# Optimization experiments

Hardware: AMD Instinct MI355X
Metric: run time of the kernel (lower is better)

## Reference

```python
import jax, jax.numpy as jnp
import numpy as np

NUM_TYPES = 4
IN_DIM = 128
HID_DIM = 256
OUT_DIM = 128
NUM_NODES = 100000


def setup_inputs() -> dict:
    key = jax.random.key(0)
    k_x, k_t, k_w1, k_b1, k_w2, k_b2 = jax.random.split(key, 6)
    raw_features = jax.random.normal(k_x, (NUM_NODES, IN_DIM), dtype=jnp.float32)
    node_type = jax.random.randint(k_t, (NUM_NODES,), 0, NUM_TYPES, dtype=jnp.int64)
    # stacked per-type MLP params (Kaiming-ish scale like torch Linear defaults)
    W1 = jax.random.uniform(k_w1, (NUM_TYPES, IN_DIM, HID_DIM), dtype=jnp.float32,
                            minval=-1.0, maxval=1.0) / np.sqrt(IN_DIM)
    b1 = jax.random.uniform(k_b1, (NUM_TYPES, HID_DIM), dtype=jnp.float32,
                            minval=-1.0, maxval=1.0) / np.sqrt(IN_DIM)
    W2 = jax.random.uniform(k_w2, (NUM_TYPES, HID_DIM, OUT_DIM), dtype=jnp.float32,
                            minval=-1.0, maxval=1.0) / np.sqrt(HID_DIM)
    b2 = jax.random.uniform(k_b2, (NUM_TYPES, OUT_DIM), dtype=jnp.float32,
                            minval=-1.0, maxval=1.0) / np.sqrt(HID_DIM)
    return {"raw_features": raw_features, "node_type": node_type,
            "W1": W1, "b1": b1, "W2": W2, "b2": b2}


def reference(raw_features, node_type, W1, b1, W2, b2):
    # Run every expert on every node (num_types is tiny), then select per node.
    # h: [types, nodes, hidden]
    h = jax.nn.relu(jnp.einsum('ni,tih->tnh', raw_features, W1) + b1[:, None, :])
    # out_all: [types, nodes, out]
    out_all = jnp.einsum('tnh,tho->tno', h, W2) + b2[:, None, :]
    # select expert output matching each node's type -> [nodes, out]
    encoded = out_all[node_type, jnp.arange(raw_features.shape[0])]
    return encoded
```

## Files before the change

### kernel.cpp

```cpp
#include <hip/hip_runtime.h>
#include <hip/hip_bf16.h>

typedef float f32x4 __attribute__((ext_vector_type(4)));
typedef short short8 __attribute__((ext_vector_type(8)));

#define NTYPES 4


static __device__ __forceinline__ unsigned short f2bf(float f) {
  union { float f; unsigned int u; } v; v.f = f;
  unsigned int u = v.u;
  unsigned int r = u + 0x7FFFu + ((u >> 16) & 1u);
  return (unsigned short)(r >> 16);
}

static __device__ __forceinline__ unsigned int pkbf(float a, float b) {
  __hip_bfloat162 h = __float22bfloat162_rn(make_float2(a, b));
  union { __hip_bfloat162 h; unsigned int u; } v; v.h = h;
  return v.u;
}

__global__ __launch_bounds__(256) void k_prep(const float* __restrict__ W1,
                                              const float* __restrict__ W2,
                                              unsigned short* __restrict__ W1T,
                                              unsigned short* __restrict__ W2T,
                                              int* __restrict__ meta) {
  __shared__ unsigned short s[64][72];
  const int tid = threadIdx.x;
  const int b = blockIdx.x;
  if (b == 0 && tid < 16) meta[tid] = 0;
  const int bb = b & 31;
  const int t = bb >> 3, ti = bb & 7;
  const float* src; unsigned short* dst; int scols, tr, tc;
  if (b < 32) { src = W1 + t * 32768; dst = W1T + t * 32768; scols = 256; tr = ti >> 2; tc = ti & 3; }
  else        { src = W2 + t * 32768; dst = W2T + t * 32768; scols = 128; tr = ti >> 1; tc = ti & 1; }
  const int srows = 32768 / scols;
  const int r0 = tid >> 4, c4 = (tid & 15) << 2;
  #pragma unroll
  for (int i = 0; i < 4; ++i) {
    int r = tr * 64 + i * 16 + r0;
    float4 v = *(const float4*)(src + r * scols + tc * 64 + c4);
    s[i * 16 + r0][c4 + 0] = f2bf(v.x);
    s[i * 16 + r0][c4 + 1] = f2bf(v.y);
    s[i * 16 + r0][c4 + 2] = f2bf(v.z);
    s[i * 16 + r0][c4 + 3] = f2bf(v.w);
  }
  __syncthreads();
  #pragma unroll
  for (int i = 0; i < 4; ++i) {
    int orow = i * 16 + r0;
    ushort4 u;
    u.x = s[c4 + 0][orow];
    u.y = s[c4 + 1][orow];
    u.z = s[c4 + 2][orow];
    u.w = s[c4 + 3][orow];
    *(ushort4*)(dst + (tc * 64 + orow) * srows + tr * 64 + c4) = u;
  }
}

__global__ __launch_bounds__(256) void k_hist(const int* __restrict__ NT, int n,
                                              int* __restrict__ meta) {
  __shared__ int c[NTYPES];
  if (threadIdx.x < NTYPES) c[threadIdx.x] = 0;
  __syncthreads();
  int i = blockIdx.x * 256 + threadIdx.x;
  if (i < n) atomicAdd(&c[NT[i]], 1);
  __syncthreads();
  if (threadIdx.x < NTYPES && c[threadIdx.x] > 0)
    atomicAdd(&meta[threadIdx.x], c[threadIdx.x]);
}

__global__ __launch_bounds__(256) void k_scatter(const int* __restrict__ NT, int n,
                                                 int* __restrict__ meta,
                                                 int* __restrict__ perm) {
  __shared__ int cnt[NTYPES];
  __shared__ int cbase[NTYPES];
  __shared__ int sb[NTYPES + 1];
  if (threadIdx.x < NTYPES) cnt[threadIdx.x] = 0;
  if (threadIdx.x == 0) {
    int b = 0; sb[0] = 0;
    for (int t = 0; t < NTYPES; ++t) {
      b += (meta[t] + 63) & ~63;
      sb[t + 1] = b;
    }
  }
  __syncthreads();
  int i = blockIdx.x * 256 + threadIdx.x;
  int t = 0, r = 0;
  bool valid = (i < n);
  if (valid) { t = NT[i]; r = atomicAdd(&cnt[t], 1); }
  __syncthreads();
  if (threadIdx.x < NTYPES)
    cbase[threadIdx.x] = atomicAdd(&meta[4 + threadIdx.x], cnt[threadIdx.x]);
  __syncthreads();
  if (valid) perm[sb[t] + cbase[t] + r] = i;
  if (blockIdx.x == 0) {
    if (threadIdx.x <= NTYPES) meta[8 + threadIdx.x] = sb[threadIdx.x];
    int tt = threadIdx.x >> 6, j = threadIdx.x & 63;
    int p = sb[tt] + meta[tt] + j;
    if (p < sb[tt + 1]) perm[p] = -1;
  }
}

__global__ __launch_bounds__(256, 1) void k_mlpw(
    const float* __restrict__ X, const int* __restrict__ perm,
    const int* __restrict__ meta,
    const unsigned short* __restrict__ W1T, const unsigned short* __restrict__ W2T,
    const float* __restrict__ B1, const float* __restrict__ B2,
    float* __restrict__ OUT, float* __restrict__ dump) {
  __shared__ __align__(16) unsigned char x_lds[16384];
  __shared__ __align__(16) unsigned char h_lds[32768];

  const int tid = threadIdx.x;
  const int l  = tid & 63, w = tid >> 6;
  const int lo = l & 15,  hi = l >> 4;

  const int t  = blockIdx.x >> 7;
  const int lb = blockIdx.x & 127;
  const int g0 = meta[8 + t] >> 6;
  const int g1 = meta[9 + t] >> 6;
  const int nt = g1 - g0 - lb;
  if (nt <= 0) return;
  const int cnt = (nt + 127) >> 7;

  const int gr = tid >> 2;
  const int gq = tid & 3;

  int pm = perm[(g0 + lb) * 64 + gr];
  float4 xv[8];
  #pragma unroll
  for (int i = 0; i < 8; ++i) xv[i] = make_float4(0.f, 0.f, 0.f, 0.f);
  if (pm >= 0) {
    const float4* s = (const float4*)(X + (size_t)pm * 128 + gq * 32);
    #pragma unroll
    for (int i = 0; i < 8; ++i) xv[i] = s[i];
  }

  const unsigned short* w1t = W1T + (t << 15);
  const unsigned short* w2t = W2T + (t << 15);
  short8 a1[4][4];
  #pragma unroll
  for (int ks = 0; ks < 4; ++ks)
    #pragma unroll
    for (int m = 0; m < 4; ++m)
      a1[ks][m] = *(const short8*)(w1t + (w * 64 + m * 16 + lo) * 128 + ks * 32 + hi * 8);
  short8 a2[8][2];
  #pragma unroll
  for (int ks = 0; ks < 8; ++ks)
    #pragma unroll
    for (int mo = 0; mo < 2; ++mo)
      a2[ks][mo] = *(const short8*)(w2t + (w * 32 + mo * 16 + lo) * 256 + ks * 32 + hi * 8);
  f32x4 bb1[4], bb2[2];
  #pragma unroll
  for (int m = 0; m < 4; ++m)
    bb1[m] = *(const f32x4*)(B1 + t * 256 + w * 64 + m * 16 + hi * 4);
  #pragma unroll
  for (int mo = 0; mo < 2; ++mo)
    bb2[mo] = *(const f32x4*)(B2 + t * 128 + w * 32 + mo * 16 + hi * 4);

  for (int j = 0; j < cnt; ++j) {
    const int g = g0 + lb + j * 128;
    const bool hn = (j + 1 < cnt);

    {
      const int rbase = gr * 256;
      const int swz = (gr & 7) << 4;
      #pragma unroll
      for (int q = 0; q < 4; ++q) {
        float4 va = xv[2 * q], vb = xv[2 * q + 1];
        uint4 u;
        u.x = pkbf(va.x, va.y); u.y = pkbf(va.z, va.w);
        u.z = pkbf(vb.x, vb.y); u.w = pkbf(vb.z, vb.w);
        int byte = (rbase + gq * 64 + q * 16) ^ swz;
        *(uint4*)(x_lds + byte) = u;
      }
    }
    __syncthreads();

    int pmn = -1;
    if (hn) pmn = perm[(g + 128) * 64 + gr];
    int rid[4];
    #pragma unroll
    for (int n = 0; n < 4; ++n) rid[n] = perm[g * 64 + n * 16 + lo];

    f32x4 acc[4][4];
    #pragma unroll
    for (int m = 0; m < 4; ++m)
      #pragma unroll
      for (int n = 0; n < 4; ++n) acc[m][n] = (f32x4){0.f, 0.f, 0.f, 0.f};
    #pragma unroll
    for (int ks = 0; ks < 4; ++ks) {
      short8 b[4];
      #pragma unroll
      for (int n = 0; n < 4; ++n) {
        int row = n * 16 + lo;
        int byte = (row * 256 + ks * 64 + hi * 16) ^ ((row & 7) << 4);
        b[n] = *(const short8*)(x_lds + byte);
      }
      #pragma unroll
      for (int m = 0; m < 4; ++m)
        #pragma unroll
        for (int n = 0; n < 4; ++n)
          acc[m][n] = __builtin_amdgcn_mfma_f32_16x16x32_bf16(a1[ks][m], b[n], acc[m][n], 0, 0, 0);
    }

    #pragma unroll
    for (int m = 0; m < 4; ++m) {
      const int hw2 = w * 128 + m * 32 + hi * 8;
      #pragma unroll
      for (int n = 0; n < 4; ++n) {
        int node = n * 16 + lo;
        uint2 hu;
        hu.x = pkbf(fmaxf(acc[m][n][0] + bb1[m][0], 0.f),
                    fmaxf(acc[m][n][1] + bb1[m][1], 0.f));
        hu.y = pkbf(fmaxf(acc[m][n][2] + bb1[m][2], 0.f),
                    fmaxf(acc[m][n][3] + bb1[m][3], 0.f));
        int byte = (node * 512 + hw2) ^ ((node & 7) << 4);
        *(uint2*)(h_lds + byte) = hu;
      }
    }
    __syncthreads();

    float4 nv[8];
    #pragma unroll
    for (int i = 0; i < 8; ++i) nv[i] = make_float4(0.f, 0.f, 0.f, 0.f);
    if (pmn >= 0) {
      const float4* s = (const float4*)(X + (size_t)pmn * 128 + gq * 32);
      #pragma unroll
      for (int i = 0; i < 8; ++i) nv[i] = s[i];
    }

    f32x4 acc2[2][4];
    #pragma unroll
    for (int mo = 0; mo < 2; ++mo)
      #pragma unroll
      for (int n = 0; n < 4; ++n) acc2[mo][n] = (f32x4){0.f, 0.f, 0.f, 0.f};
    #pragma unroll
    for (int ks = 0; ks < 8; ++ks) {
      short8 b[4];
      #pragma unroll
      for (int n = 0; n < 4; ++n) {
        int node = n * 16 + lo;
        int byte = (node * 512 + ks * 64 + hi * 16) ^ ((node & 7) << 4);
        b[n] = *(const short8*)(h_lds + byte);
      }
      #pragma unroll
      for (int mo = 0; mo < 2; ++mo)
        #pragma unroll
        for (int n = 0; n < 4; ++n)
          acc2[mo][n] = __builtin_amdgcn_mfma_f32_16x16x32_bf16(a2[ks][mo], b[n], acc2[mo][n], 0, 0, 0);
    }

    #pragma unroll
    for (int mo = 0; mo < 2; ++mo) {
      const int oc = w * 32 + mo * 16 + hi * 4;
      #pragma unroll
      for (int n = 0; n < 4; ++n) {
        f32x4 o = acc2[mo][n];
        o[0] += bb2[mo][0]; o[1] += bb2[mo][1];
        o[2] += bb2[mo][2]; o[3] += bb2[mo][3];
        float* dst = (rid[n] >= 0) ? (OUT + (size_t)rid[n] * 128 + oc) : (dump + oc);
        *(f32x4*)dst = o;
      }
    }

    #pragma unroll
    for (int i = 0; i < 8; ++i) xv[i] = nv[i];
  }
}

extern "C" void kernel_launch(void* const* d_in, const int* in_sizes, int n_in,
                              void* d_out, int out_size, void* d_ws, size_t ws_size,
                              hipStream_t stream) {
  const float* X  = (const float*)d_in[0];
  const int*   NT = (const int*)d_in[1];
  const float* W1 = (const float*)d_in[2];
  const float* B1 = (const float*)d_in[3];
  const float* W2 = (const float*)d_in[4];
  const float* B2 = (const float*)d_in[5];
  float* OUT = (float*)d_out;
  const int n = in_sizes[1];

  char* ws = (char*)d_ws;
  int* meta = (int*)ws;
  float* dump = (float*)(ws + 512);
  int* perm = (int*)(ws + 1024);
  unsigned short* W1T = (unsigned short*)(ws + 402432);
  unsigned short* W2T = (unsigned short*)(ws + 664576);

  k_prep<<<64, 256, 0, stream>>>(W1, W2, W1T, W2T, meta);
  const int nb = (n + 255) / 256;
  k_hist<<<nb, 256, 0, stream>>>(NT, n, meta);
  k_scatter<<<nb, 256, 0, stream>>>(NT, n, meta, perm);
  k_mlpw<<<512, 256, 0, stream>>>(X, perm, meta, W1T, W2T, B1, B2, OUT, dump);
}
```

Baseline: 61.29 us.

## Coalesce gathered X loads and stage outputs through LDS for row-contiguous stores

Row indices for the next tile are prefetched into a double-buffered shared array. X is gathered with 32 threads covering one full 512-byte row per load, replacing per-thread 128-byte strided chunks. The layer-2 outputs are written to LDS and read back so each scattered output row is stored by a contiguous group of threads, instead of MFMA-layout 16-byte fragments. This improves global coalescing on both the gather and the scatter, at the cost of two extra barriers and an LDS round trip per tile.

```diff
diff --git a/kernel.cpp b/kernel.cpp
--- a/kernel.cpp
+++ b/kernel.cpp
@@ -110,10 +110,13 @@
     float* __restrict__ OUT, float* __restrict__ dump) {
   __shared__ __align__(16) unsigned char x_lds[16384];
   __shared__ __align__(16) unsigned char h_lds[32768];
+  __shared__ int s_rid[2][64];
 
   const int tid = threadIdx.x;
   const int l  = tid & 63, w = tid >> 6;
   const int lo = l & 15,  hi = l >> 4;
+  const int rg = tid >> 5;
+  const int c4 = (tid & 31) * 4;
 
   const int t  = blockIdx.x >> 7;
   const int lb = blockIdx.x & 127;
@@ -123,17 +126,15 @@
   if (nt <= 0) return;
   const int cnt = (nt + 127) >> 7;
 
-  const int gr = tid >> 2;
-  const int gq = tid & 3;
-
-  int pm = perm[(g0 + lb) * 64 + gr];
+  if (tid < 64) s_rid[0][tid] = perm[(g0 + lb) * 64 + tid];
+  __syncthreads();
   float4 xv[8];
   #pragma unroll
-  for (int i = 0; i < 8; ++i) xv[i] = make_float4(0.f, 0.f, 0.f, 0.f);
-  if (pm >= 0) {
-    const float4* s = (const float4*)(X + (size_t)pm * 128 + gq * 32);
-    #pragma unroll
-    for (int i = 0; i < 8; ++i) xv[i] = s[i];
+  for (int p = 0; p < 8; ++p) {
+    int row = p * 8 + rg;
+    int rd = s_rid[0][row];
+    xv[p] = make_float4(0.f, 0.f, 0.f, 0.f);
+    if (rd >= 0) xv[p] = *(const float4*)(X + (size_t)rd * 128 + c4);
   }
 
   const unsigned short* w1t = W1T + (t << 15);
@@ -161,27 +162,20 @@
   for (int j = 0; j < cnt; ++j) {
     const int g = g0 + lb + j * 128;
     const bool hn = (j + 1 < cnt);
-
-    {
-      const int rbase = gr * 256;
-      const int swz = (gr & 7) << 4;
-      #pragma unroll
-      for (int q = 0; q < 4; ++q) {
-        float4 va = xv[2 * q], vb = xv[2 * q + 1];
-        uint4 u;
-        u.x = pkbf(va.x, va.y); u.y = pkbf(va.z, va.w);
-        u.z = pkbf(vb.x, vb.y); u.w = pkbf(vb.z, vb.w);
-        int byte = (rbase + gq * 64 + q * 16) ^ swz;
-        *(uint4*)(x_lds + byte) = u;
-      }
+    const int cur = j & 1, nxt = cur ^ 1;
+
+    #pragma unroll
+    for (int p = 0; p < 8; ++p) {
+      int row = p * 8 + rg;
+      uint2 u;
+      u.x = pkbf(xv[p].x, xv[p].y);
+      u.y = pkbf(xv[p].z, xv[p].w);
+      int byte = (row * 256 + c4 * 2) ^ ((row & 7) << 4);
+      *(uint2*)(x_lds + byte) = u;
     }
     __syncthreads();
 
-    int pmn = -1;
-    if (hn) pmn = perm[(g + 128) * 64 + gr];
-    int rid[4];
-    #pragma unroll
-    for (int n = 0; n < 4; ++n) rid[n] = perm[g * 64 + n * 16 + lo];
+    if (hn && tid < 64) s_rid[nxt][tid] = perm[(g + 128) * 64 + tid];
 
     f32x4 acc[4][4];
     #pragma unroll
@@ -223,11 +217,13 @@
 
     float4 nv[8];
     #pragma unroll
-    for (int i = 0; i < 8; ++i) nv[i] = make_float4(0.f, 0.f, 0.f, 0.f);
-    if (pmn >= 0) {
-      const float4* s = (const float4*)(X + (size_t)pmn * 128 + gq * 32);
-      #pragma unroll
-      for (int i = 0; i < 8; ++i) nv[i] = s[i];
+    for (int p = 0; p < 8; ++p) nv[p] = make_float4(0.f, 0.f, 0.f, 0.f);
+    if (hn) {
+      #pragma unroll
+      for (int p = 0; p < 8; ++p) {
+        int rd = s_rid[nxt][p * 8 + rg];
+        if (rd >= 0) nv[p] = *(const float4*)(X + (size_t)rd * 128 + c4);
+      }
     }
 
     f32x4 acc2[2][4];
@@ -250,22 +246,34 @@
         for (int n = 0; n < 4; ++n)
           acc2[mo][n] = __builtin_amdgcn_mfma_f32_16x16x32_bf16(a2[ks][mo], b[n], acc2[mo][n], 0, 0, 0);
     }
+    __syncthreads();
 
     #pragma unroll
     for (int mo = 0; mo < 2; ++mo) {
       const int oc = w * 32 + mo * 16 + hi * 4;
       #pragma unroll
       for (int n = 0; n < 4; ++n) {
+        int node = n * 16 + lo;
         f32x4 o = acc2[mo][n];
         o[0] += bb2[mo][0]; o[1] += bb2[mo][1];
         o[2] += bb2[mo][2]; o[3] += bb2[mo][3];
-        float* dst = (rid[n] >= 0) ? (OUT + (size_t)rid[n] * 128 + oc) : (dump + oc);
-        *(f32x4*)dst = o;
-      }
-    }
-
-    #pragma unroll
-    for (int i = 0; i < 8; ++i) xv[i] = nv[i];
+        int byte = (node * 512 + oc * 4) ^ ((node & 7) << 4);
+        *(f32x4*)(h_lds + byte) = o;
+      }
+    }
+    __syncthreads();
+
+    #pragma unroll
+    for (int p = 0; p < 8; ++p) {
+      int row = p * 8 + rg;
+      int rd = s_rid[cur][row];
+      f32x4 v = *(const f32x4*)(h_lds + ((row * 512 + c4 * 4) ^ ((row & 7) << 4)));
+      float* dst = (rd >= 0) ? (OUT + (size_t)rd * 128 + c4) : (dump + c4);
+      *(f32x4*)dst = v;
+    }
+
+    #pragma unroll
+    for (int p = 0; p < 8; ++p) xv[p] = nv[p];
   }
 }
 
```

New measurement: 58.45 us. -4.6%, faster.
